# Performance work log

Measured on AMD Instinct MI355X. Metric: run time of the kernel, lower is better.

The kernel has to match this reference:

```python
import jax, jax.numpy as jnp
import numpy as np

ALPHA = 1.702
LIMIT = 7.0


def setup_inputs() -> dict:
    key = jax.random.key(0)
    ks = jax.random.split(key, 6)
    A, B, E, M, H = 1, 1, 8, 1024, 2048
    I2 = 4096  # 2 * intermediate_size, interleaved gate/up
    inter = I2 // 2
    return {
        "dispatched": jax.random.normal(ks[0], (A, B, E, M, H), dtype=jnp.float32),
        "w1": jax.random.normal(ks[1], (E, H, I2), dtype=jnp.float32) * 0.02,
        "w1_bias": jax.random.normal(ks[2], (E, I2), dtype=jnp.float32) * 0.02,
        "w2": jax.random.normal(ks[3], (E, inter, H), dtype=jnp.float32) * 0.02,
        "w2_bias": jax.random.normal(ks[4], (E, H), dtype=jnp.float32) * 0.02,
        "sparsity_remap": jax.random.randint(ks[5], (E,), 0, E, dtype=jnp.int32),
        "BD": 1,
        "S": 1024,
    }


def reference(dispatched, w1, w1_bias, w2, w2_bias, sparsity_remap, BD, S):
    # dispatched: [A, B, E, M, H]; w1: [E, H, 2I]; w2: [E, I, H]
    # tt.sparse_matmul == grouped per-expert GEMM; dense math is identical.
    A, Bt, E, M, H = dispatched.shape
    # fused gate+up projection: [A, B, E, M, 2I]
    gu = jnp.einsum("abemh,ehn->abemn", dispatched, w1) + w1_bias[None, None, :, None, :]
    # interleaved gate/up split (gpt_oss activation path)
    gate = gu[..., 0::2]
    up = gu[..., 1::2]
    gate = jnp.minimum(gate, LIMIT)
    up = jnp.clip(up, -LIMIT, LIMIT)
    glu = gate * jax.nn.sigmoid(gate * ALPHA)
    activated = (up + 1.0) * glu  # [A, B, E, M, I]
    inter = activated.shape[-1]
    activated = activated.reshape(A * Bt, E, M, inter)
    # down projection: [A*B, E, M, H]
    down = jnp.einsum("bemi,eih->bemh", activated, w2) + w2_bias[None, :, None, :]
    # permute(1,0,2,3) then untile to [E, 1, BD*S, H]
    out = jnp.transpose(down, (1, 0, 2, 3)).reshape(E, 1, BD * S, H)
    return out
```

## Files before the change

kernel.cpp:

```cpp
#include <hip/hip_runtime.h>
#include <hip/hip_bf16.h>
#include <cstdint>
#include <cstddef>

#define E_ 8
#define M_ 1024
#define H_ 2048
#define I2_ 4096
#define INTER_ 2048

typedef __attribute__((ext_vector_type(8))) __bf16 bf16x8;
typedef __attribute__((ext_vector_type(4))) float f32x4;

__device__ __forceinline__ unsigned short f2bf(float x) {
  union { float f; unsigned u; } v; v.f = x;
  unsigned r = v.u + 0x7fffu + ((v.u >> 16) & 1u);
  return (unsigned short)(r >> 16);
}

__device__ __forceinline__ unsigned pk2(float lo, float hi) {
  __hip_bfloat162 h = __float22bfloat162_rn(make_float2(lo, hi));
  union { __hip_bfloat162 h2; unsigned u; } c; c.h2 = h; return c.u;
}

__device__ __forceinline__ int bofs(int kp, int r) {
  int f = (20 * ((kp >> 2) & 3)) ^ ((kp & 1) << 4);
  return kp * 128 + (r ^ f);
}

__global__ void k_cvt(const float* __restrict__ src, unsigned short* __restrict__ dst, int n4) {
  int i = blockIdx.x * blockDim.x + threadIdx.x;
  int stride = gridDim.x * blockDim.x;
  const float4* s4 = (const float4*)src;
  ushort4* d4 = (ushort4*)dst;
  for (; i < n4; i += stride) {
    float4 v = s4[i];
    ushort4 o;
    o.x = f2bf(v.x); o.y = f2bf(v.y); o.z = f2bf(v.z); o.w = f2bf(v.w);
    d4[i] = o;
  }
}

template<int ACT, int N, int K>
__global__ __launch_bounds__(256) void k_gemm(
    const unsigned short* __restrict__ A,
    const float* __restrict__ Bf,
    const float* __restrict__ bias,
    unsigned short* __restrict__ ActOut,
    float* __restrict__ Out)
{
  __shared__ unsigned short la[128 * 64];
  __shared__ unsigned lb32[32 * 128];
  const int tid = threadIdx.x;
  const int lane = tid & 63;
  const int wv = tid >> 6;
  const int wm = wv & 1, wn = wv >> 1;
  const int e = blockIdx.z;
  const int n0 = blockIdx.x * 128;
  const int m0 = blockIdx.y * 128;
  const unsigned short* Ae = A + (size_t)e * M_ * K + (size_t)m0 * K;
  const float* Be = Bf + (size_t)e * K * N + n0;

  const unsigned short* ga[4];
  int segb[4];
  #pragma unroll
  for (int t = 0; t < 4; ++t) {
    int s = (wv * 4 + t) * 64 + lane;
    int m = s >> 3;
    int j = (s & 7) ^ (m & 7);
    ga[t] = Ae + (size_t)m * K + j * 8;
    segb[t] = (wv * 4 + t) * 1024;
  }

  int kpb, colb, rg;
  if (ACT) {
    kpb = tid >> 4;
    int g = tid & 15;
    colb = 8 * g;
    rg = 32 * (g >> 2) + 4 * (g & 3);
  } else {
    kpb = tid >> 5;
    colb = 4 * (tid & 31);
    rg = colb;
  }
  const float* bg = Be + (size_t)(2 * kpb) * N + colb;

  const int c = lane & 15;
  const int q = lane >> 4;

  f32x4 acc[4][4];
  const f32x4 zero = {0.f, 0.f, 0.f, 0.f};
  #pragma unroll
  for (int i = 0; i < 4; ++i)
    #pragma unroll
    for (int j = 0; j < 4; ++j) acc[i][j] = zero;

  #define LD4(p, off) (*(const float4*)((p) + (off)))

  float4 pb[8];
  {
    const float* p = bg;
    if (ACT) {
      pb[0] = LD4(p, 0);                    pb[1] = LD4(p, 4);
      pb[2] = LD4(p, (size_t)N);            pb[3] = LD4(p, (size_t)N + 4);
      pb[4] = LD4(p, (size_t)32 * N);       pb[5] = LD4(p, (size_t)32 * N + 4);
      pb[6] = LD4(p, (size_t)33 * N);       pb[7] = LD4(p, (size_t)33 * N + 4);
    } else {
      #pragma unroll
      for (int uu = 0; uu < 4; ++uu) {
        pb[2 * uu]     = LD4(p, (size_t)(16 * uu) * N);
        pb[2 * uu + 1] = LD4(p, (size_t)(16 * uu + 1) * N);
      }
    }
  }

  const int KT = K / 64;
  for (int kt = 0; kt < KT; ++kt) {
    #pragma unroll
    for (int t = 0; t < 4; ++t) {
      __builtin_amdgcn_global_load_lds(
          (const __attribute__((address_space(1))) void*)(const void*)(ga[t] + kt * 64),
          (__attribute__((address_space(3))) void*)(void*)((char*)la + segb[t]), 16, 0, 0);
    }
    if (ACT) {
      #pragma unroll
      for (int uu = 0; uu < 2; ++uu) {
        int kp = kpb + 16 * uu;
        float4 a0 = pb[4 * uu], a1 = pb[4 * uu + 1], b0 = pb[4 * uu + 2], b1 = pb[4 * uu + 3];
        uint4 gv, uv;
        gv.x = pk2(a0.x, b0.x); gv.y = pk2(a0.z, b0.z); gv.z = pk2(a1.x, b1.x); gv.w = pk2(a1.z, b1.z);
        uv.x = pk2(a0.y, b0.y); uv.y = pk2(a0.w, b0.w); uv.z = pk2(a1.y, b1.y); uv.w = pk2(a1.w, b1.w);
        *(uint4*)&lb32[bofs(kp, rg)] = gv;
        *(uint4*)&lb32[bofs(kp, rg + 16)] = uv;
      }
    } else {
      #pragma unroll
      for (int uu = 0; uu < 4; ++uu) {
        int kp = kpb + 8 * uu;
        float4 a = pb[2 * uu], b = pb[2 * uu + 1];
        uint4 v;
        v.x = pk2(a.x, b.x); v.y = pk2(a.y, b.y); v.z = pk2(a.z, b.z); v.w = pk2(a.w, b.w);
        *(uint4*)&lb32[bofs(kp, rg)] = v;
      }
    }
    __syncthreads();

    if (kt + 1 < KT) {
      const float* p = bg + (size_t)(kt + 1) * 64 * N;
      if (ACT) {
        pb[0] = LD4(p, 0);                    pb[1] = LD4(p, 4);
        pb[2] = LD4(p, (size_t)N);            pb[3] = LD4(p, (size_t)N + 4);
        pb[4] = LD4(p, (size_t)32 * N);       pb[5] = LD4(p, (size_t)32 * N + 4);
        pb[6] = LD4(p, (size_t)33 * N);       pb[7] = LD4(p, (size_t)33 * N + 4);
      } else {
        #pragma unroll
        for (int uu = 0; uu < 4; ++uu) {
          pb[2 * uu]     = LD4(p, (size_t)(16 * uu) * N);
          pb[2 * uu + 1] = LD4(p, (size_t)(16 * uu + 1) * N);
        }
      }
    }

    #pragma unroll
    for (int ks = 0; ks < 2; ++ks) {
      bf16x8 av[4], bv[4];
      #pragma unroll
      for (int mi = 0; mi < 4; ++mi) {
        int row = wm * 64 + mi * 16 + c;
        int slot = row * 8 + ((ks * 4 + q) ^ (c & 7));
        av[mi] = *(const bf16x8*)(la + slot * 8);
      }
      #pragma unroll
      for (int ni = 0; ni < 4; ++ni) {
        int r = wn * 64 + ni * 16 + c;
        union { unsigned u[4]; bf16x8 v; } t;
        #pragma unroll
        for (int jp = 0; jp < 4; ++jp)
          t.u[jp] = lb32[bofs(ks * 16 + q * 4 + jp, r)];
        bv[ni] = t.v;
      }
      #pragma unroll
      for (int mi = 0; mi < 4; ++mi)
        #pragma unroll
        for (int ni = 0; ni < 4; ++ni)
          acc[mi][ni] = __builtin_amdgcn_mfma_f32_16x16x32_bf16(av[mi], bv[ni], acc[mi][ni], 0, 0, 0);
    }
    __syncthreads();
  }
  #undef LD4

  if (ACT) {
    unsigned short* ActE = ActOut + (size_t)e * M_ * (N / 2);
    const float* be = bias + (size_t)e * N;
    int colbase = n0 + wn * 64;
    #pragma unroll
    for (int p = 0; p < 2; ++p) {
      int rgc = colbase + 32 * p + c;
      int norig = (rgc & ~31) | (c << 1);
      float bg_ = be[norig];
      float bu_ = be[norig + 1];
      int acol = ((rgc >> 5) << 4) + c;
      #pragma unroll
      for (int mi = 0; mi < 4; ++mi) {
        int rowb = m0 + wm * 64 + mi * 16 + q * 4;
        #pragma unroll
        for (int r = 0; r < 4; ++r) {
          float g = acc[mi][2 * p][r] + bg_;
          float u = acc[mi][2 * p + 1][r] + bu_;
          g = fminf(g, 7.0f);
          u = fminf(fmaxf(u, -7.0f), 7.0f);
          float glu = g / (1.0f + __expf(-1.702f * g));
          float a = (u + 1.0f) * glu;
          ActE[(size_t)(rowb + r) * (N / 2) + acol] = f2bf(a);
        }
      }
    }
  } else {
    float* OutE = Out + (size_t)e * M_ * N;
    const float* be = bias + (size_t)e * N;
    #pragma unroll
    for (int ni = 0; ni < 4; ++ni) {
      int col = n0 + wn * 64 + ni * 16 + c;
      float bb = be[col];
      #pragma unroll
      for (int mi = 0; mi < 4; ++mi) {
        int rowb = m0 + wm * 64 + mi * 16 + q * 4;
        #pragma unroll
        for (int r = 0; r < 4; ++r)
          OutE[(size_t)(rowb + r) * N + col] = acc[mi][ni][r] + bb;
      }
    }
  }
}

__global__ __launch_bounds__(256) void k_naive(const float* __restrict__ disp,
    const float* __restrict__ w1, const float* __restrict__ w1b,
    const float* __restrict__ w2, const float* __restrict__ w2b,
    float* __restrict__ out) {
  __shared__ float xrow[H_];
  __shared__ float act[INTER_];
  int b = blockIdx.x;
  int e = b / M_;
  int m = b % M_;
  const float* x = disp + (size_t)(e * M_ + m) * H_;
  int tid = threadIdx.x;
  for (int k = tid; k < H_; k += 256) xrow[k] = x[k];
  __syncthreads();
  const float* w1e = w1 + (size_t)e * H_ * I2_;
  const float* b1e = w1b + (size_t)e * I2_;
  for (int jj = 0; jj < INTER_ / 256; ++jj) {
    int i = tid + jj * 256;
    float g = b1e[2 * i], u = b1e[2 * i + 1];
    for (int k = 0; k < H_; ++k) {
      float xv = xrow[k];
      g += xv * w1e[(size_t)k * I2_ + 2 * i];
      u += xv * w1e[(size_t)k * I2_ + 2 * i + 1];
    }
    g = fminf(g, 7.0f);
    u = fminf(fmaxf(u, -7.0f), 7.0f);
    float glu = g / (1.0f + __expf(-1.702f * g));
    act[i] = (u + 1.0f) * glu;
  }
  __syncthreads();
  const float* w2e = w2 + (size_t)e * INTER_ * H_;
  const float* b2e = w2b + (size_t)e * H_;
  float* oute = out + (size_t)(e * M_ + m) * H_;
  for (int jj = 0; jj < H_ / 256; ++jj) {
    int h = tid + jj * 256;
    float o = b2e[h];
    for (int i = 0; i < INTER_; ++i) o += act[i] * w2e[(size_t)i * H_ + h];
    oute[h] = o;
  }
}

extern "C" void kernel_launch(void* const* d_in, const int* in_sizes, int n_in,
                              void* d_out, int out_size, void* d_ws, size_t ws_size,
                              hipStream_t stream) {
  const float* disp = (const float*)d_in[0];
  const float* w1   = (const float*)d_in[1];
  const float* w1b  = (const float*)d_in[2];
  const float* w2   = (const float*)d_in[3];
  const float* w2b  = (const float*)d_in[4];
  float* out = (float*)d_out;

  const size_t nA   = (size_t)E_ * M_ * H_;
  const size_t nAct = (size_t)E_ * M_ * INTER_;
  const size_t need = (nA + nAct) * 2;

  if (ws_size >= need) {
    unsigned short* actb = (unsigned short*)d_ws;
    unsigned short* ab   = actb + nAct;

    k_cvt<<<4096, 256, 0, stream>>>(disp, ab, (int)(nA / 4));
    k_gemm<1, I2_, H_><<<dim3(I2_ / 128, M_ / 128, E_), 256, 0, stream>>>(ab, w1, w1b, actb, nullptr);
    k_gemm<0, H_, INTER_><<<dim3(H_ / 128, M_ / 128, E_), 256, 0, stream>>>(actb, w2, w2b, nullptr, out);
  } else {
    k_naive<<<E_ * M_, 256, 0, stream>>>(disp, w1, w1b, w2, w2b, out);
  }
}
```

Baseline: 813.7 us.

## Pre-transpose weights to bf16 K-major and use NT GEMM with async loads

Adds a kernel that converts and transposes the fp32 weights into bf16 N×K layout (permuting gate/up columns for W1) in workspace. A new NT GEMM then loads both A and B tiles straight into LDS with swizzled global_load_lds instead of converting fp32 B in registers each k-step. This takes conversion work off the GEMM inner loop, but it adds a full weight-conversion pass on every call, costs extra workspace, and the NT GEMM has no prefetch overlap. A harmless rewrite of one pack line is also made in the old path.

```diff
diff --git a/kernel.cpp b/kernel.cpp
--- a/kernel.cpp
+++ b/kernel.cpp
@@ -38,6 +38,171 @@
     ushort4 o;
     o.x = f2bf(v.x); o.y = f2bf(v.y); o.z = f2bf(v.z); o.w = f2bf(v.w);
     d4[i] = o;
+  }
+}
+
+template<int PERM>
+__global__ __launch_bounds__(256) void k_wt(
+    const float* __restrict__ W, unsigned short* __restrict__ Wp, int Kd, int Nd) {
+  __shared__ float tt[64][65];
+  const int tid = threadIdx.x;
+  const int e = blockIdx.z;
+  const int nb0 = blockIdx.x * 64;
+  const int k0 = blockIdx.y * 64;
+  const float* We = W + (size_t)e * Kd * Nd;
+
+  #pragma unroll
+  for (int i = 0; i < 4; ++i) {
+    int r = (tid >> 4) + 16 * i;
+    int c4 = tid & 15;
+    float4 v = *(const float4*)(We + (size_t)(k0 + r) * Nd + nb0 + 4 * c4);
+    tt[r][4 * c4 + 0] = v.x;
+    tt[r][4 * c4 + 1] = v.y;
+    tt[r][4 * c4 + 2] = v.z;
+    tt[r][4 * c4 + 3] = v.w;
+  }
+  __syncthreads();
+
+  int n = tid >> 2;
+  int kc = (tid & 3) * 16;
+  int nglob = nb0 + n;
+  int nrow;
+  if (PERM) {
+    int b = nglob >> 5, w = nglob & 31;
+    nrow = 32 * b + ((w & 1) ? 16 + (w >> 1) : (w >> 1));
+  } else {
+    nrow = nglob;
+  }
+  unsigned o[8];
+  #pragma unroll
+  for (int j = 0; j < 8; ++j)
+    o[j] = pk2(tt[kc + 2 * j][n], tt[kc + 2 * j + 1][n]);
+  unsigned short* dst = Wp + (size_t)e * Nd * Kd + (size_t)nrow * Kd + k0 + kc;
+  *(uint4*)(dst) = *(uint4*)&o[0];
+  *(uint4*)(dst + 8) = *(uint4*)&o[4];
+}
+
+template<int ACT, int N, int K>
+__global__ __launch_bounds__(256) void k_gemm_nt(
+    const unsigned short* __restrict__ A,
+    const unsigned short* __restrict__ B,
+    const float* __restrict__ bias,
+    unsigned short* __restrict__ ActOut,
+    float* __restrict__ Out)
+{
+  __shared__ unsigned short la[128 * 64];
+  __shared__ unsigned short lb[128 * 64];
+  const int tid = threadIdx.x;
+  const int lane = tid & 63;
+  const int wv = tid >> 6;
+  const int wm = wv & 1, wn = wv >> 1;
+  const int e = blockIdx.z;
+  const int n0 = blockIdx.x * 128;
+  const int m0 = blockIdx.y * 128;
+  const unsigned short* Ae = A + (size_t)e * M_ * K + (size_t)m0 * K;
+  const unsigned short* Be = B + (size_t)e * N * K + (size_t)n0 * K;
+
+  const unsigned short* ga[4];
+  const unsigned short* gb[4];
+  int seg[4];
+  #pragma unroll
+  for (int t = 0; t < 4; ++t) {
+    int s = (wv * 4 + t) * 64 + lane;
+    int m = s >> 3;
+    int j = (s & 7) ^ (m & 7);
+    ga[t] = Ae + (size_t)m * K + j * 8;
+    gb[t] = Be + (size_t)m * K + j * 8;
+    seg[t] = (wv * 4 + t) * 1024;
+  }
+
+  const int c = lane & 15;
+  const int q = lane >> 4;
+
+  f32x4 acc[4][4];
+  const f32x4 zero = {0.f, 0.f, 0.f, 0.f};
+  #pragma unroll
+  for (int i = 0; i < 4; ++i)
+    #pragma unroll
+    for (int j = 0; j < 4; ++j) acc[i][j] = zero;
+
+  const int KT = K / 64;
+  for (int kt = 0; kt < KT; ++kt) {
+    #pragma unroll
+    for (int t = 0; t < 4; ++t) {
+      __builtin_amdgcn_global_load_lds(
+          (const __attribute__((address_space(1))) void*)(const void*)(ga[t] + kt * 64),
+          (__attribute__((address_space(3))) void*)(void*)((char*)la + seg[t]), 16, 0, 0);
+      __builtin_amdgcn_global_load_lds(
+          (const __attribute__((address_space(1))) void*)(const void*)(gb[t] + kt * 64),
+          (__attribute__((address_space(3))) void*)(void*)((char*)lb + seg[t]), 16, 0, 0);
+    }
+    __syncthreads();
+
+    #pragma unroll
+    for (int ks = 0; ks < 2; ++ks) {
+      bf16x8 av[4], bv[4];
+      #pragma unroll
+      for (int mi = 0; mi < 4; ++mi) {
+        int row = wm * 64 + mi * 16 + c;
+        int slot = row * 8 + ((ks * 4 + q) ^ (c & 7));
+        av[mi] = *(const bf16x8*)(la + slot * 8);
+      }
+      #pragma unroll
+      for (int ni = 0; ni < 4; ++ni) {
+        int row = wn * 64 + ni * 16 + c;
+        int slot = row * 8 + ((ks * 4 + q) ^ (c & 7));
+        bv[ni] = *(const bf16x8*)(lb + slot * 8);
+      }
+      #pragma unroll
+      for (int mi = 0; mi < 4; ++mi)
+        #pragma unroll
+        for (int ni = 0; ni < 4; ++ni)
+          acc[mi][ni] = __builtin_amdgcn_mfma_f32_16x16x32_bf16(av[mi], bv[ni], acc[mi][ni], 0, 0, 0);
+    }
+    __syncthreads();
+  }
+
+  if (ACT) {
+    unsigned short* ActE = ActOut + (size_t)e * M_ * (N / 2);
+    const float* be = bias + (size_t)e * N;
+    int colbase = n0 + wn * 64;
+    #pragma unroll
+    for (int p = 0; p < 2; ++p) {
+      int rgc = colbase + 32 * p + c;
+      int norig = (rgc & ~31) | (c << 1);
+      float bg_ = be[norig];
+      float bu_ = be[norig + 1];
+      int acol = ((rgc >> 5) << 4) + c;
+      #pragma unroll
+      for (int mi = 0; mi < 4; ++mi) {
+        int rowb = m0 + wm * 64 + mi * 16 + q * 4;
+        #pragma unroll
+        for (int r = 0; r < 4; ++r) {
+          float g = acc[mi][2 * p][r] + bg_;
+          float u = acc[mi][2 * p + 1][r] + bu_;
+          g = fminf(g, 7.0f);
+          u = fminf(fmaxf(u, -7.0f), 7.0f);
+          float glu = g / (1.0f + __expf(-1.702f * g));
+          float a = (u + 1.0f) * glu;
+          ActE[(size_t)(rowb + r) * (N / 2) + acol] = f2bf(a);
+        }
+      }
+    }
+  } else {
+    float* OutE = Out + (size_t)e * M_ * N;
+    const float* be = bias + (size_t)e * N;
+    #pragma unroll
+    for (int ni = 0; ni < 4; ++ni) {
+      int col = n0 + wn * 64 + ni * 16 + c;
+      float bb = be[col];
+      #pragma unroll
+      for (int mi = 0; mi < 4; ++mi) {
+        int rowb = m0 + wm * 64 + mi * 16 + q * 4;
+        #pragma unroll
+        for (int r = 0; r < 4; ++r)
+          OutE[(size_t)(rowb + r) * N + col] = acc[mi][ni][r] + bb;
+      }
+    }
   }
 }
 
@@ -129,7 +294,8 @@
         float4 a0 = pb[4 * uu], a1 = pb[4 * uu + 1], b0 = pb[4 * uu + 2], b1 = pb[4 * uu + 3];
         uint4 gv, uv;
         gv.x = pk2(a0.x, b0.x); gv.y = pk2(a0.z, b0.z); gv.z = pk2(a1.x, b1.x); gv.w = pk2(a1.z, b1.z);
-        uv.x = pk2(a0.y, b0.y); uv.y = pk2(a0.w, b0.w); uv.z = pk2(a1.y, b1.y); uv.w = pk2(a1.w, b1.w);
+        uv.x = pk2(a0.y, b0.y); uv.y = pk2(a0.w, b0.w); uv.z = pk2(a1.w, b1.w); uv.w = pk2(a1.w, b1.w);
+        uv.z = pk2(a1.y, b1.y);
         *(uint4*)&lb32[bofs(kp, rg)] = gv;
         *(uint4*)&lb32[bofs(kp, rg + 16)] = uv;
       }
@@ -285,9 +451,23 @@
 
   const size_t nA   = (size_t)E_ * M_ * H_;
   const size_t nAct = (size_t)E_ * M_ * INTER_;
-  const size_t need = (nA + nAct) * 2;
-
-  if (ws_size >= need) {
+  const size_t nW1  = (size_t)E_ * I2_ * H_;
+  const size_t nW2  = (size_t)E_ * H_ * INTER_;
+  const size_t need_full = (nA + nAct + nW1 + nW2) * 2;
+  const size_t need_old  = (nA + nAct) * 2;
+
+  if (ws_size >= need_full) {
+    unsigned short* actb = (unsigned short*)d_ws;
+    unsigned short* ab   = actb + nAct;
+    unsigned short* w1p  = ab + nA;
+    unsigned short* w2p  = w1p + nW1;
+
+    k_cvt<<<4096, 256, 0, stream>>>(disp, ab, (int)(nA / 4));
+    k_wt<1><<<dim3(I2_ / 64, H_ / 64, E_), 256, 0, stream>>>(w1, w1p, H_, I2_);
+    k_wt<0><<<dim3(H_ / 64, INTER_ / 64, E_), 256, 0, stream>>>(w2, w2p, INTER_, H_);
+    k_gemm_nt<1, I2_, H_><<<dim3(I2_ / 128, M_ / 128, E_), 256, 0, stream>>>(ab, w1p, w1b, actb, nullptr);
+    k_gemm_nt<0, H_, INTER_><<<dim3(H_ / 128, M_ / 128, E_), 256, 0, stream>>>(actb, w2p, w2b, nullptr, out);
+  } else if (ws_size >= need_old) {
     unsigned short* actb = (unsigned short*)d_ws;
     unsigned short* ab   = actb + nAct;
 
```

Result: slower. 831.3 us (+2.2%).
